# Performance work log

Hardware: AMD Instinct MI355X
Metric: run time of the kernel (lower is better)

The kernel has to match this reference:

```python
import jax, jax.numpy as jnp
import numpy as np

EMBED = 1024
HEAD = 64

def setup_inputs() -> dict:
    key = jax.random.key(0)
    k1, k2, k3, k4 = jax.random.split(key, 4)
    embeddings = jax.random.normal(k1, (8, 2048, EMBED), dtype=jnp.float32)
    # nn.Linear weight is [out, in]; we store transposed [in, out] for x @ W
    scale = 1.0 / np.sqrt(EMBED)
    Wk = jax.random.uniform(k2, (EMBED, HEAD), dtype=jnp.float32, minval=-scale, maxval=scale)
    Wq = jax.random.uniform(k3, (EMBED, HEAD), dtype=jnp.float32, minval=-scale, maxval=scale)
    Wv = jax.random.uniform(k4, (EMBED, HEAD), dtype=jnp.float32, minval=-scale, maxval=scale)
    return {"embeddings": embeddings, "Wq": Wq, "Wk": Wk, "Wv": Wv}

def reference(embeddings, Wq, Wk, Wv):
    B, S, D = embeddings.shape
    q = embeddings @ Wq  # [B,S,H]
    k = embeddings @ Wk
    v = embeddings @ Wv
    norm = k.shape[-1] ** (-0.5)
    scores = jnp.einsum('bqh,bkh->bqk', q, k) * norm  # [B,S,S]
    causal = jnp.tril(jnp.ones((S, S), dtype=bool))
    scores = jnp.where(causal, scores, -jnp.inf)
    weights = jax.nn.softmax(scores, axis=-1)
    # dropout p=0.0 (eval-equivalent): identity
    return jnp.einsum('bqk,bkh->bqh', weights, v)
```

## Files before the change

### kernel.cpp

```cpp
#include <hip/hip_runtime.h>

#define SEQ   2048
#define NBATCH 8
#define EMB   1024
#define HD    64
#define QKVSZ (NBATCH * SEQ * HD)
#define WTSZ  (3 * HD * EMB)
#define PSLOT2 4224

typedef __attribute__((ext_vector_type(8))) short bf16x8;
typedef __attribute__((ext_vector_type(4))) float f32x4;

__device__ inline unsigned short f2b(float f) {
  union { float f; unsigned int i; } u; u.f = f;
  unsigned int r = (u.i + 0x7FFFu + ((u.i >> 16) & 1u)) >> 16;
  return (unsigned short)r;
}

#define GLOAD_LDS16(g, l)                                              \
  __builtin_amdgcn_global_load_lds(                                    \
      (const __attribute__((address_space(1))) void*)(g),              \
      (__attribute__((address_space(3))) void*)(l), 16, 0, 0)

__global__ __launch_bounds__(256) void wtrans_kernel(const float* __restrict__ wq,
                                                     const float* __restrict__ wk,
                                                     const float* __restrict__ wv,
                                                     unsigned short* __restrict__ wt) {
  int i = blockIdx.x * 256 + threadIdx.x;
  int kb  = i / 12288;
  int rem = i - kb * 12288;
  int m   = rem >> 12;
  int c   = (rem >> 6) & 63;
  int kd  = rem & 63;
  const float* src = (m == 0) ? wq : ((m == 1) ? wk : wv);
  int d = kb * 64 + kd;
  wt[i] = f2b(src[d * 64 + c]);
}

__global__ __launch_bounds__(256, 4) void qkv_proj_kernel(const float* __restrict__ emb,
                                                          const unsigned short* __restrict__ wt,
                                                          unsigned short* __restrict__ qkv) {
  __shared__ __align__(16) unsigned short Ab[2][32 * 64];
  __shared__ __align__(16) unsigned short Wb[2][96 * 64];

  const int t    = threadIdx.x;
  const int wave = t >> 6;
  const int lane = t & 63;
  const int quad = lane >> 4;
  const int l16  = lane & 15;
  const int bx = blockIdx.x;
  const int rt = ((bx >> 4) << 3) | (bx & 7);
  const int ch = (bx >> 3) & 1;
  const int wr = wave >> 1;
  const int wc = wave & 1;

  const float* aBase = emb + (size_t)rt * 32 * EMB;
  const char*  wChunk = (const char*)(wt + ch * 6144);

  int wsrc[3];
#pragma unroll
  for (int i = 0; i < 3; i++) {
    int u = (wave * 3 + i) * 64 + lane;
    int row = u >> 3, k8 = u & 7;
    wsrc[i] = row * 128 + ((k8 ^ (row & 7)) << 4);
  }

  f32x4 acc[3];
#pragma unroll
  for (int j = 0; j < 3; j++) acc[j] = (f32x4){0.f, 0.f, 0.f, 0.f};
  f32x4 pa[2];

#define QKVA_ISSUE(kb)                                                              \
  do {                                                                              \
    _Pragma("unroll") for (int j = 0; j < 2; j++) {                                 \
      int u = t + j * 256;                                                          \
      pa[j] = *(const f32x4*)(aBase + (size_t)(u >> 4) * EMB + (kb) * 64 + (u & 15) * 4); \
    }                                                                               \
  } while (0)

#define QKVW_DMA(kb, buf)                                                           \
  do {                                                                              \
    _Pragma("unroll") for (int i = 0; i < 3; i++)                                   \
      GLOAD_LDS16(wChunk + (size_t)(kb) * 24576 + wsrc[i],                          \
                  (char*)&Wb[buf][0] + (wave * 3 + i) * 1024);                      \
  } while (0)

#define QKVA_STAGE(buf)                                                             \
  do {                                                                              \
    _Pragma("unroll") for (int j = 0; j < 2; j++) {                                 \
      int u = t + j * 256;                                                          \
      int row = u >> 4, kq = u & 15;                                                \
      unsigned int lo = (unsigned int)f2b(pa[j][0]) | ((unsigned int)f2b(pa[j][1]) << 16); \
      unsigned int hi = (unsigned int)f2b(pa[j][2]) | ((unsigned int)f2b(pa[j][3]) << 16); \
      uint2 pk; pk.x = lo; pk.y = hi;                                               \
      *(uint2*)((char*)&Ab[buf][0] + row * 128 + ((kq * 8) ^ ((row & 7) << 4))) = pk; \
    }                                                                               \
  } while (0)

#define QKV_COMPUTE(buf)                                                            \
  do {                                                                              \
    const int arow = wr * 16 + l16;                                                 \
    _Pragma("unroll") for (int kh = 0; kh < 2; kh++) {                              \
      bf16x8 af = *(const bf16x8*)((const char*)&Ab[buf][0] + arow * 128 +          \
                                   ((kh * 64 + quad * 16) ^ ((arow & 7) << 4)));    \
      _Pragma("unroll") for (int j = 0; j < 3; j++) {                               \
        const int coll = (wc * 3 + j) * 16 + l16;                                   \
        bf16x8 wf = *(const bf16x8*)((const char*)&Wb[buf][0] + coll * 128 +        \
                                     ((kh * 64 + quad * 16) ^ ((coll & 7) << 4)));  \
        acc[j] = __builtin_amdgcn_mfma_f32_16x16x32_bf16(af, wf, acc[j], 0, 0, 0);  \
      }                                                                             \
    }                                                                               \
  } while (0)

  QKVA_ISSUE(0);
  QKVW_DMA(0, 0);
  QKVA_STAGE(0);
  __syncthreads();

  for (int kb = 0; kb < 16; kb++) {
    const int cur = kb & 1;
    const int nb  = cur ^ 1;
    if (kb < 15) {
      QKVA_ISSUE(kb + 1);
      QKVW_DMA(kb + 1, nb);
    }
    QKV_COMPUTE(cur);
    if (kb < 15) QKVA_STAGE(nb);
    __syncthreads();
  }

#pragma unroll
  for (int j = 0; j < 3; j++) {
    int gc = ch * 96 + (wc * 3 + j) * 16 + l16;
    if (gc < 128) {
      int m  = gc >> 6, cm = gc & 63;
#pragma unroll
      for (int r = 0; r < 4; r++) {
        int row = rt * 32 + wr * 16 + quad * 4 + r;
        qkv[(size_t)m * QKVSZ + (size_t)row * HD + cm] = f2b(acc[j][r]);
      }
    }
  }

  if (ch == 1) {
    __syncthreads();
    unsigned short* Vsh = (unsigned short*)&Ab[0][0];
#pragma unroll
    for (int j = 0; j < 3; j++) {
      int gc = 96 + (wc * 3 + j) * 16 + l16;
      if (gc >= 128) {
        int h = gc - 128;
#pragma unroll
        for (int r = 0; r < 4; r++)
          Vsh[h * 40 + wr * 16 + quad * 4 + r] = f2b(acc[j][r]);
      }
    }
    __syncthreads();
    int h  = t >> 2;
    int sq = (t & 3) * 8;
    int row0 = rt * 32;
    int b    = row0 >> 11;
    int seq0 = row0 & 2047;
    bf16x8 vv = *(const bf16x8*)(Vsh + h * 40 + sq);
    *(bf16x8*)(qkv + 2 * (size_t)QKVSZ + ((size_t)(b * 64 + h)) * SEQ + seq0 + sq) = vv;
  }
}

__global__ __launch_bounds__(256, 4) void attn_split(const unsigned short* __restrict__ qkv,
                                                     float* __restrict__ part,
                                                     float* __restrict__ out) {
  __shared__ __align__(16) unsigned short Kb[2][64 * 64];
  __shared__ __align__(16) unsigned short Vb[2][64 * 64];
  __shared__ __align__(16) unsigned short Pb[4][16 * 64];

  const int t    = threadIdx.x;
  const int wave = t >> 6;
  const int lane = t & 63;
  const int quad = lane >> 4;
  const int l16  = lane & 15;
  const int B0 = blockIdx.x;
  const int c  = blockIdx.y;
  const int b  = blockIdx.z;
  const int nch = (B0 >> 3) + 1;
  if (c >= nch) return;
  const int t0 = c * 8;
  const int t1 = min(t0 + 7, B0);
  const int qt = B0 * 4 + wave;
  const int q0 = qt * 16;

  const unsigned short* qg = qkv;
  const unsigned short* kg = qkv + QKVSZ;
  const unsigned short* vg = qkv + 2 * QKVSZ;

  const unsigned short* qptr = qg + ((size_t)(b * SEQ + q0 + l16)) * HD + quad * 8;
  const bf16x8 qf0 = *(const bf16x8*)qptr;
  const bf16x8 qf1 = *(const bf16x8*)(qptr + 32);

  int koff[2]; size_t voff[2];
#pragma unroll
  for (int i = 0; i < 2; i++) {
    int u = (wave * 2 + i) * 64 + lane;
    int row = u >> 3, k8 = u & 7;
    int swz = (k8 ^ (row & 7)) << 4;
    koff[i] = row * 128 + swz;
    voff[i] = ((size_t)(b * 64 + row) * SEQ) * 2 + swz;
  }
  const char* kgB = (const char*)kg + (size_t)b * SEQ * 128;
  const char* vgB = (const char*)vg;

  f32x4 o0 = {0,0,0,0}, o1 = {0,0,0,0}, o2 = {0,0,0,0}, o3 = {0,0,0,0};
  float mst[4] = {-INFINITY, -INFINITY, -INFINITY, -INFINITY};
  float lst[4] = {0.f, 0.f, 0.f, 0.f};
  const float sc = 0.125f * 1.44269504088896f;

#pragma unroll
  for (int i = 0; i < 2; i++) {
    GLOAD_LDS16(kgB + (size_t)t0 * 8192 + koff[i], (char*)&Kb[0][0] + (wave * 2 + i) * 1024);
    GLOAD_LDS16(vgB + voff[i] + (size_t)t0 * 128,  (char*)&Vb[0][0] + (wave * 2 + i) * 1024);
  }
  __syncthreads();

  for (int kb = t0; kb <= t1; kb++) {
    const int cur = (kb - t0) & 1;
    const int nb  = cur ^ 1;

    if (kb < t1) {
#pragma unroll
      for (int i = 0; i < 2; i++) {
        GLOAD_LDS16(kgB + (size_t)(kb + 1) * 8192 + koff[i], (char*)&Kb[nb][0] + (wave * 2 + i) * 1024);
        GLOAD_LDS16(vgB + voff[i] + (size_t)(kb + 1) * 128,  (char*)&Vb[nb][0] + (wave * 2 + i) * 1024);
      }
    }

    f32x4 s[4];
#pragma unroll
    for (int kt = 0; kt < 4; kt++) {
      int row = kt * 16 + l16;
      bf16x8 kf0 = *(const bf16x8*)((char*)&Kb[cur][0] + row * 128 + ((quad * 16) ^ ((row & 7) << 4)));
      bf16x8 kf1 = *(const bf16x8*)((char*)&Kb[cur][0] + row * 128 + ((64 + quad * 16) ^ ((row & 7) << 4)));
      f32x4 z = {0.f, 0.f, 0.f, 0.f};
      z = __builtin_amdgcn_mfma_f32_16x16x32_bf16(qf0, kf0, z, 0, 0, 0);
      z = __builtin_amdgcn_mfma_f32_16x16x32_bf16(qf1, kf1, z, 0, 0, 0);
      s[kt] = z;
    }

    if (kb == B0) {
#pragma unroll
      for (int r = 0; r < 4; r++) {
        int rowg = q0 + quad * 4 + r;
#pragma unroll
        for (int kt = 0; kt < 4; kt++) {
          int col = kb * 64 + kt * 16 + l16;
          float v = s[kt][r] * sc;
          s[kt][r] = (col > rowg) ? -INFINITY : v;
        }
      }
    } else {
#pragma unroll
      for (int r = 0; r < 4; r++)
#pragma unroll
        for (int kt = 0; kt < 4; kt++) s[kt][r] *= sc;
    }

    float alpha[4];
#pragma unroll
    for (int r = 0; r < 4; r++) {
      float mx = fmaxf(fmaxf(s[0][r], s[1][r]), fmaxf(s[2][r], s[3][r]));
#pragma unroll
      for (int off = 1; off < 16; off <<= 1) mx = fmaxf(mx, __shfl_xor(mx, off, 64));
      float mnew = fmaxf(mst[r], mx);
      alpha[r] = exp2f(mst[r] - mnew);
      mst[r] = mnew;
    }
#pragma unroll
    for (int r = 0; r < 4; r++) {
      float sm = 0.f;
#pragma unroll
      for (int kt = 0; kt < 4; kt++) {
        float p = exp2f(s[kt][r] - mst[r]);
        s[kt][r] = p;
        sm += p;
      }
#pragma unroll
      for (int off = 1; off < 16; off <<= 1) sm += __shfl_xor(sm, off, 64);
      lst[r] = lst[r] * alpha[r] + sm;
    }
#pragma unroll
    for (int r = 0; r < 4; r++) { o0[r] *= alpha[r]; o1[r] *= alpha[r]; o2[r] *= alpha[r]; o3[r] *= alpha[r]; }

#pragma unroll
    for (int kt = 0; kt < 4; kt++)
#pragma unroll
      for (int r = 0; r < 4; r++) {
        int row = quad * 4 + r;
        *(unsigned short*)((char*)&Pb[wave][0] + row * 128 +
                           ((kt * 32 + l16 * 2) ^ ((row & 7) << 4))) = f2b(s[kt][r]);
      }

#pragma unroll
    for (int kc = 0; kc < 2; kc++) {
      bf16x8 pf = *(const bf16x8*)((char*)&Pb[wave][0] + l16 * 128 +
                                   ((kc * 64 + quad * 16) ^ ((l16 & 7) << 4)));
      int r0 = l16, r1 = 16 + l16, r2 = 32 + l16, r3 = 48 + l16;
      bf16x8 vf0 = *(const bf16x8*)((char*)&Vb[cur][0] + r0 * 128 + ((kc * 64 + quad * 16) ^ ((r0 & 7) << 4)));
      bf16x8 vf1 = *(const bf16x8*)((char*)&Vb[cur][0] + r1 * 128 + ((kc * 64 + quad * 16) ^ ((r1 & 7) << 4)));
      bf16x8 vf2 = *(const bf16x8*)((char*)&Vb[cur][0] + r2 * 128 + ((kc * 64 + quad * 16) ^ ((r2 & 7) << 4)));
      bf16x8 vf3 = *(const bf16x8*)((char*)&Vb[cur][0] + r3 * 128 + ((kc * 64 + quad * 16) ^ ((r3 & 7) << 4)));
      o0 = __builtin_amdgcn_mfma_f32_16x16x32_bf16(pf, vf0, o0, 0, 0, 0);
      o1 = __builtin_amdgcn_mfma_f32_16x16x32_bf16(pf, vf1, o1, 0, 0, 0);
      o2 = __builtin_amdgcn_mfma_f32_16x16x32_bf16(pf, vf2, o2, 0, 0, 0);
      o3 = __builtin_amdgcn_mfma_f32_16x16x32_bf16(pf, vf3, o3, 0, 0, 0);
    }

    __syncthreads();
  }

  if (nch == 1) {
#pragma unroll
    for (int r = 0; r < 4; r++) {
      float inv = 1.f / lst[r];
      int rowg = q0 + quad * 4 + r;
      size_t ob = ((size_t)(b * SEQ + rowg)) * HD + l16;
      out[ob + 0]  = o0[r] * inv;
      out[ob + 16] = o1[r] * inv;
      out[ob + 32] = o2[r] * inv;
      out[ob + 48] = o3[r] * inv;
    }
  } else {
    float* ps = part + ((size_t)((b * 32 + B0) * 4 + c)) * PSLOT2;
#pragma unroll
    for (int r = 0; r < 4; r++) {
      int row = wave * 16 + quad * 4 + r;
      ps[row * 64 + 0  + l16] = o0[r];
      ps[row * 64 + 16 + l16] = o1[r];
      ps[row * 64 + 32 + l16] = o2[r];
      ps[row * 64 + 48 + l16] = o3[r];
      if (l16 == 0) {
        ps[4096 + row] = mst[r];
        ps[4160 + row] = lst[r];
      }
    }
  }
}

__global__ __launch_bounds__(256) void attn_merge(const float* __restrict__ part,
                                                  float* __restrict__ out) {
  const int bx = blockIdx.x;
  const int B0 = 8 + (bx >> 2);
  const int rg = bx & 3;
  const int b  = blockIdx.y;
  const int nch = (B0 >> 3) + 1;
  const int t  = threadIdx.x;
  const int h  = t & 63;
  const int rloc = t >> 6;
  const float* base = part + ((size_t)((b * 32 + B0) * 4)) * PSLOT2;
#pragma unroll
  for (int i = 0; i < 4; i++) {
    int row = rg * 16 + rloc * 4 + i;
    float mv[4], lv[4], ov[4];
#pragma unroll
    for (int cc = 0; cc < 4; cc++) {
      int cs = (cc < nch) ? cc : 0;
      const float* ps = base + (size_t)cs * PSLOT2;
      mv[cc] = ps[4096 + row];
      lv[cc] = ps[4160 + row];
      ov[cc] = ps[row * 64 + h];
    }
    float M = -INFINITY;
#pragma unroll
    for (int cc = 0; cc < 4; cc++) M = fmaxf(M, (cc < nch) ? mv[cc] : -INFINITY);
    float L = 0.f, o = 0.f;
#pragma unroll
    for (int cc = 0; cc < 4; cc++) {
      float e = (cc < nch) ? exp2f(mv[cc] - M) : 0.f;
      L += lv[cc] * e;
      o += ov[cc] * e;
    }
    out[((size_t)(b * SEQ + B0 * 64 + row)) * HD + h] = o / L;
  }
}

extern "C" void kernel_launch(void* const* d_in, const int* in_sizes, int n_in,
                              void* d_out, int out_size, void* d_ws, size_t ws_size,
                              hipStream_t stream) {
  const float* emb = (const float*)d_in[0];
  const float* wq  = (const float*)d_in[1];
  const float* wk  = (const float*)d_in[2];
  const float* wv  = (const float*)d_in[3];
  unsigned short* ws  = (unsigned short*)d_ws;
  unsigned short* wt  = ws;
  unsigned short* qkv = ws + WTSZ;
  float* part = (float*)(ws + WTSZ + 3 * QKVSZ);

  hipLaunchKernelGGL(wtrans_kernel,   dim3(WTSZ / 256), dim3(256), 0, stream, wq, wk, wv, wt);
  hipLaunchKernelGGL(qkv_proj_kernel, dim3(1024),       dim3(256), 0, stream, emb, wt, qkv);
  hipLaunchKernelGGL(attn_split,      dim3(32, 4, 8),   dim3(256), 0, stream, qkv, part, (float*)d_out);
  hipLaunchKernelGGL(attn_merge,      dim3(96, 8),      dim3(256), 0, stream, part, (float*)d_out);
}
```

Measured before the change: 151.2 us.

## Compute all QKV columns per block to read embeddings only once

Restructures the QKV projection so each 192-thread block computes all 192 output columns (Q, K, V) for its 32 rows, instead of splitting columns across two blocks. This halves the global reads of the fp32 embedding tensor. In exchange, the block holds a larger weight tile in LDS, uses fewer blocks, and may run at lower occupancy.

Measured after the change: 151.5 us. About the same (+0.2%).

```diff
diff --git a/kernel.cpp b/kernel.cpp
--- a/kernel.cpp
+++ b/kernel.cpp
@@ -37,77 +37,82 @@
   wt[i] = f2b(src[d * 64 + c]);
 }
 
-__global__ __launch_bounds__(256, 4) void qkv_proj_kernel(const float* __restrict__ emb,
-                                                          const unsigned short* __restrict__ wt,
-                                                          unsigned short* __restrict__ qkv) {
+__global__ __launch_bounds__(192) void qkv_proj_kernel(const float* __restrict__ emb,
+                                                       const unsigned short* __restrict__ wt,
+                                                       unsigned short* __restrict__ qkv) {
   __shared__ __align__(16) unsigned short Ab[2][32 * 64];
-  __shared__ __align__(16) unsigned short Wb[2][96 * 64];
+  __shared__ __align__(16) unsigned short Wb[2][192 * 64];
 
   const int t    = threadIdx.x;
   const int wave = t >> 6;
   const int lane = t & 63;
   const int quad = lane >> 4;
   const int l16  = lane & 15;
-  const int bx = blockIdx.x;
-  const int rt = ((bx >> 4) << 3) | (bx & 7);
-  const int ch = (bx >> 3) & 1;
-  const int wr = wave >> 1;
-  const int wc = wave & 1;
+  const int rt   = blockIdx.x;
 
   const float* aBase = emb + (size_t)rt * 32 * EMB;
-  const char*  wChunk = (const char*)(wt + ch * 6144);
-
-  int wsrc[3];
-#pragma unroll
-  for (int i = 0; i < 3; i++) {
-    int u = (wave * 3 + i) * 64 + lane;
+  const char*  wBase = (const char*)wt;
+
+  int wsrc[8];
+#pragma unroll
+  for (int i = 0; i < 8; i++) {
+    int u = (wave * 8 + i) * 64 + lane;
     int row = u >> 3, k8 = u & 7;
     wsrc[i] = row * 128 + ((k8 ^ (row & 7)) << 4);
   }
 
-  f32x4 acc[3];
-#pragma unroll
-  for (int j = 0; j < 3; j++) acc[j] = (f32x4){0.f, 0.f, 0.f, 0.f};
-  f32x4 pa[2];
+  f32x4 acc[2][4];
+#pragma unroll
+  for (int a = 0; a < 2; a++)
+#pragma unroll
+    for (int n = 0; n < 4; n++) acc[a][n] = (f32x4){0.f, 0.f, 0.f, 0.f};
+  f32x4 pa[3];
 
 #define QKVA_ISSUE(kb)                                                              \
   do {                                                                              \
-    _Pragma("unroll") for (int j = 0; j < 2; j++) {                                 \
-      int u = t + j * 256;                                                          \
-      pa[j] = *(const f32x4*)(aBase + (size_t)(u >> 4) * EMB + (kb) * 64 + (u & 15) * 4); \
+    _Pragma("unroll") for (int j = 0; j < 3; j++) {                                 \
+      int u = t + j * 192;                                                          \
+      if (j < 2 || t < 128)                                                         \
+        pa[j] = *(const f32x4*)(aBase + (size_t)(u >> 4) * EMB + (kb) * 64 + (u & 15) * 4); \
     }                                                                               \
   } while (0)
 
 #define QKVW_DMA(kb, buf)                                                           \
   do {                                                                              \
-    _Pragma("unroll") for (int i = 0; i < 3; i++)                                   \
-      GLOAD_LDS16(wChunk + (size_t)(kb) * 24576 + wsrc[i],                          \
-                  (char*)&Wb[buf][0] + (wave * 3 + i) * 1024);                      \
+    _Pragma("unroll") for (int i = 0; i < 8; i++)                                   \
+      GLOAD_LDS16(wBase + (size_t)(kb) * 24576 + wsrc[i],                           \
+                  (char*)&Wb[buf][0] + (wave * 8 + i) * 1024);                      \
   } while (0)
 
 #define QKVA_STAGE(buf)                                                             \
   do {                                                                              \
-    _Pragma("unroll") for (int j = 0; j < 2; j++) {                                 \
-      int u = t + j * 256;                                                          \
-      int row = u >> 4, kq = u & 15;                                                \
-      unsigned int lo = (unsigned int)f2b(pa[j][0]) | ((unsigned int)f2b(pa[j][1]) << 16); \
-      unsigned int hi = (unsigned int)f2b(pa[j][2]) | ((unsigned int)f2b(pa[j][3]) << 16); \
-      uint2 pk; pk.x = lo; pk.y = hi;                                               \
-      *(uint2*)((char*)&Ab[buf][0] + row * 128 + ((kq * 8) ^ ((row & 7) << 4))) = pk; \
+    _Pragma("unroll") for (int j = 0; j < 3; j++) {                                 \
+      int u = t + j * 192;                                                          \
+      if (j < 2 || t < 128) {                                                       \
+        int row = u >> 4, kq = u & 15;                                              \
+        unsigned int lo = (unsigned int)f2b(pa[j][0]) | ((unsigned int)f2b(pa[j][1]) << 16); \
+        unsigned int hi = (unsigned int)f2b(pa[j][2]) | ((unsigned int)f2b(pa[j][3]) << 16); \
+        uint2 pk; pk.x = lo; pk.y = hi;                                             \
+        *(uint2*)((char*)&Ab[buf][0] + row * 128 + ((kq * 8) ^ ((row & 7) << 4))) = pk; \
+      }                                                                             \
     }                                                                               \
   } while (0)
 
 #define QKV_COMPUTE(buf)                                                            \
   do {                                                                              \
-    const int arow = wr * 16 + l16;                                                 \
     _Pragma("unroll") for (int kh = 0; kh < 2; kh++) {                              \
-      bf16x8 af = *(const bf16x8*)((const char*)&Ab[buf][0] + arow * 128 +          \
-                                   ((kh * 64 + quad * 16) ^ ((arow & 7) << 4)));    \
-      _Pragma("unroll") for (int j = 0; j < 3; j++) {                               \
-        const int coll = (wc * 3 + j) * 16 + l16;                                   \
-        bf16x8 wf = *(const bf16x8*)((const char*)&Wb[buf][0] + coll * 128 +        \
-                                     ((kh * 64 + quad * 16) ^ ((coll & 7) << 4)));  \
-        acc[j] = __builtin_amdgcn_mfma_f32_16x16x32_bf16(af, wf, acc[j], 0, 0, 0);  \
+      bf16x8 af[2];                                                                 \
+      _Pragma("unroll") for (int a = 0; a < 2; a++) {                               \
+        int arow = a * 16 + l16;                                                    \
+        af[a] = *(const bf16x8*)((const char*)&Ab[buf][0] + arow * 128 +            \
+                                 ((kh * 64 + quad * 16) ^ ((arow & 7) << 4)));      \
+      }                                                                             \
+      _Pragma("unroll") for (int nt = 0; nt < 4; nt++) {                            \
+        int wrow = wave * 64 + nt * 16 + l16;                                       \
+        bf16x8 wf = *(const bf16x8*)((const char*)&Wb[buf][0] + wrow * 128 +        \
+                                     ((kh * 64 + quad * 16) ^ ((wrow & 7) << 4)));  \
+        _Pragma("unroll") for (int a = 0; a < 2; a++)                               \
+          acc[a][nt] = __builtin_amdgcn_mfma_f32_16x16x32_bf16(af[a], wf, acc[a][nt], 0, 0, 0); \
       }                                                                             \
     }                                                                               \
   } while (0)
@@ -129,40 +134,44 @@
     __syncthreads();
   }
 
-#pragma unroll
-  for (int j = 0; j < 3; j++) {
-    int gc = ch * 96 + (wc * 3 + j) * 16 + l16;
-    if (gc < 128) {
-      int m  = gc >> 6, cm = gc & 63;
-#pragma unroll
-      for (int r = 0; r < 4; r++) {
-        int row = rt * 32 + wr * 16 + quad * 4 + r;
-        qkv[(size_t)m * QKVSZ + (size_t)row * HD + cm] = f2b(acc[j][r]);
-      }
-    }
-  }
-
-  if (ch == 1) {
+  if (wave < 2) {
+#pragma unroll
+    for (int a = 0; a < 2; a++)
+#pragma unroll
+      for (int nt = 0; nt < 4; nt++)
+#pragma unroll
+        for (int r = 0; r < 4; r++) {
+          int row = rt * 32 + a * 16 + quad * 4 + r;
+          int cm  = nt * 16 + l16;
+          qkv[(size_t)wave * QKVSZ + (size_t)row * HD + cm] = f2b(acc[a][nt][r]);
+        }
+  }
+
+  __syncthreads();
+  {
+    unsigned short* Vsh = (unsigned short*)&Ab[0][0];
+    if (wave == 2) {
+#pragma unroll
+      for (int a = 0; a < 2; a++)
+#pragma unroll
+        for (int nt = 0; nt < 4; nt++)
+#pragma unroll
+          for (int r = 0; r < 4; r++)
+            Vsh[(nt * 16 + l16) * 48 + a * 16 + quad * 4 + r] = f2b(acc[a][nt][r]);
+    }
     __syncthreads();
-    unsigned short* Vsh = (unsigned short*)&Ab[0][0];
-#pragma unroll
-    for (int j = 0; j < 3; j++) {
-      int gc = 96 + (wc * 3 + j) * 16 + l16;
-      if (gc >= 128) {
-        int h = gc - 128;
-#pragma unroll
-        for (int r = 0; r < 4; r++)
-          Vsh[h * 40 + wr * 16 + quad * 4 + r] = f2b(acc[j][r]);
-      }
-    }
-    __syncthreads();
-    int h  = t >> 2;
-    int sq = (t & 3) * 8;
-    int row0 = rt * 32;
-    int b    = row0 >> 11;
-    int seq0 = row0 & 2047;
-    bf16x8 vv = *(const bf16x8*)(Vsh + h * 40 + sq);
-    *(bf16x8*)(qkv + 2 * (size_t)QKVSZ + ((size_t)(b * 64 + h)) * SEQ + seq0 + sq) = vv;
+    const int b    = rt >> 6;
+    const int seq0 = (rt & 63) * 32;
+#pragma unroll
+    for (int j = 0; j < 2; j++) {
+      int u = t + j * 192;
+      if (u < 256) {
+        int h  = u >> 2;
+        int sq = (u & 3) * 8;
+        bf16x8 vv = *(const bf16x8*)(Vsh + h * 48 + sq);
+        *(bf16x8*)(qkv + 2 * (size_t)QKVSZ + ((size_t)(b * 64 + h)) * SEQ + seq0 + sq) = vv;
+      }
+    }
   }
 }
 
@@ -393,7 +402,7 @@
   float* part = (float*)(ws + WTSZ + 3 * QKVSZ);
 
   hipLaunchKernelGGL(wtrans_kernel,   dim3(WTSZ / 256), dim3(256), 0, stream, wq, wk, wv, wt);
-  hipLaunchKernelGGL(qkv_proj_kernel, dim3(1024),       dim3(256), 0, stream, emb, wt, qkv);
+  hipLaunchKernelGGL(qkv_proj_kernel, dim3(512),        dim3(192), 0, stream, emb, wt, qkv);
   hipLaunchKernelGGL(attn_split,      dim3(32, 4, 8),   dim3(256), 0, stream, qkv, part, (float*)d_out);
   hipLaunchKernelGGL(attn_merge,      dim3(96, 8),      dim3(256), 0, stream, part, (float*)d_out);
 }
```
